# Optimization experiments

Measured on AMD Instinct MI355X. Metric: run time of the kernel, lower is better.

The kernel has to match this reference:

```python
import jax, jax.numpy as jnp
import numpy as np

E, D, H, O, K = 8, 1024, 4096, 1024, 2
N = 4096


def setup_inputs() -> dict:
    key = jax.random.key(0)
    ks = jax.random.split(key, 8)
    s_in = 1.0 / np.sqrt(D)
    s_h = 1.0 / np.sqrt(H)
    return {
        "x": jax.random.normal(ks[0], (N, D), dtype=jnp.float32),
        "W1": jax.random.uniform(ks[1], (E, D, H), jnp.float32, -s_in, s_in),
        "b1": jax.random.uniform(ks[2], (E, H), jnp.float32, -s_in, s_in),
        "W2": jax.random.uniform(ks[3], (E, H, O), jnp.float32, -s_h, s_h),
        "b2": jax.random.uniform(ks[4], (E, O), jnp.float32, -s_h, s_h),
        "Wg": jax.random.uniform(ks[5], (D, E), jnp.float32, -s_in, s_in),
        "bg": jax.random.uniform(ks[6], (E,), jnp.float32, -s_in, s_in),
    }


def reference(x, W1, b1, W2, b2, Wg, bg):
    # gate: [N, E] -> top-k logits and expert ids
    gate_logits = x @ Wg + bg
    topv, topi = jax.lax.top_k(gate_logits, K)          # [N, K]
    weights = jax.nn.softmax(topv, axis=-1)             # softmax over the k selected logits

    # dense all-expert MLP, then gather the selected experts per token
    h = jax.nn.relu(jnp.einsum("nd,edh->enh", x, W1) + b1[:, None, :])  # [E, N, H]
    y = jnp.einsum("enh,eho->eno", h, W2) + b2[:, None, :]              # [E, N, O]

    sel = y[topi, jnp.arange(N)[:, None]]               # [N, K, O]
    return jnp.sum(weights[..., None] * sel, axis=1)    # [N, O]
```

## Files before the change

### kernel.cpp

```cpp
#include <hip/hip_runtime.h>
#include <hip/hip_bf16.h>
#include <cstdint>

typedef __bf16 bf16;
typedef bf16 bf16x8 __attribute__((ext_vector_type(8)));
typedef bf16 bf16x4 __attribute__((ext_vector_type(4)));
typedef float f32x4 __attribute__((ext_vector_type(4)));

#define N_TOK 4096
#define DIM   1024
#define HID   4096
#define OUTD  1024
#define NEXP  8

__device__ __forceinline__ void async_copy16(const void* g, void* l) {
  __builtin_amdgcn_global_load_lds(
      (const __attribute__((address_space(1))) void*)g,
      (__attribute__((address_space(3))) void*)l, 16, 0, 0);
}

__global__ __launch_bounds__(256) void gate_kernel(
    const float* __restrict__ x, const float* __restrict__ Wg,
    const float* __restrict__ bg, int* __restrict__ topE, float* __restrict__ topW)
{
  int wave = threadIdx.x >> 6, lane = threadIdx.x & 63;
  int t = blockIdx.x * 4 + wave;
  float acc[8];
#pragma unroll
  for (int e = 0; e < 8; ++e) acc[e] = 0.f;
  const float* xrow = x + (size_t)t * DIM;
#pragma unroll
  for (int i = 0; i < DIM / 64; ++i) {
    int d = i * 64 + lane;
    float xv = xrow[d];
    float4 w0 = *(const float4*)(Wg + d * 8);
    float4 w1 = *(const float4*)(Wg + d * 8 + 4);
    acc[0] += xv * w0.x; acc[1] += xv * w0.y; acc[2] += xv * w0.z; acc[3] += xv * w0.w;
    acc[4] += xv * w1.x; acc[5] += xv * w1.y; acc[6] += xv * w1.z; acc[7] += xv * w1.w;
  }
#pragma unroll
  for (int off = 32; off > 0; off >>= 1) {
#pragma unroll
    for (int e = 0; e < 8; ++e) acc[e] += __shfl_xor(acc[e], off, 64);
  }
  if (lane == 0) {
    float l[8];
#pragma unroll
    for (int e = 0; e < 8; ++e) l[e] = acc[e] + bg[e];
    int e1 = 0;
#pragma unroll
    for (int e = 1; e < 8; ++e) if (l[e] > l[e1]) e1 = e;
    int e2 = (e1 == 0) ? 1 : 0;
#pragma unroll
    for (int e = 0; e < 8; ++e) if (e != e1 && l[e] > l[e2]) e2 = e;
    float w1 = 1.f / (1.f + __expf(l[e2] - l[e1]));
    topE[t * 2] = e1; topE[t * 2 + 1] = e2;
    topW[t * 2] = w1; topW[t * 2 + 1] = 1.f - w1;
  }
}

__global__ __launch_bounds__(256) void build_lists(
    const int* __restrict__ topE, const float* __restrict__ topW,
    int* __restrict__ cnt, int* __restrict__ tok_list, float* __restrict__ w_list,
    int* __restrict__ inv)
{
  __shared__ int lcnt[8], lbase[8];
  int tid = threadIdx.x;
  if (tid < 8) lcnt[tid] = 0;
  __syncthreads();
  int t = blockIdx.x * 256 + tid;
  int e1 = topE[2 * t], e2 = topE[2 * t + 1];
  float w1 = topW[2 * t], w2 = topW[2 * t + 1];
  int p1 = atomicAdd(&lcnt[e1], 1);
  int p2 = atomicAdd(&lcnt[e2], 1);
  __syncthreads();
  if (tid < 8) lbase[tid] = atomicAdd(&cnt[tid], lcnt[tid]);
  __syncthreads();
  int i1 = e1 * N_TOK + lbase[e1] + p1;
  int i2 = e2 * N_TOK + lbase[e2] + p2;
  tok_list[i1] = t; w_list[i1] = w1;
  tok_list[i2] = t; w_list[i2] = w2;
  inv[2 * t] = i1;
  inv[2 * t + 1] = i2;
}

__global__ void scan_kernel(const int* __restrict__ cnt, int* __restrict__ base)
{
  if (threadIdx.x == 0) {
    int s = 0;
    for (int e = 0; e < 8; ++e) { base[e] = s; s += cnt[e]; }
    base[8] = s;
  }
}

__global__ __launch_bounds__(256) void gather_cvt(
    const float* __restrict__ x, const int* __restrict__ tok_list,
    const int* __restrict__ base, bf16* __restrict__ xg)
{
  int wave = threadIdx.x >> 6, lane = threadIdx.x & 63;
  int s = blockIdx.x * 4 + wave;
  int e = 0;
#pragma unroll
  for (int i = 1; i < 8; ++i) e += (s >= base[i]);
  int tok = tok_list[e * N_TOK + (s - base[e])];
  const float4* src = (const float4*)(x + (size_t)tok * DIM);
  bf16x4* dst = (bf16x4*)(xg + (size_t)s * DIM);
#pragma unroll
  for (int i = 0; i < DIM / 256; ++i) {
    float4 v = src[i * 64 + lane];
    bf16x4 o;
    o.x = (bf16)v.x; o.y = (bf16)v.y; o.z = (bf16)v.z; o.w = (bf16)v.w;
    dst[i * 64 + lane] = o;
  }
}

__global__ __launch_bounds__(256) void transpose_cvt(
    const float* __restrict__ src, bf16* __restrict__ dst, int R, int C)
{
  __shared__ bf16 tile[64][65];
  int e = blockIdx.z;
  const float* s = src + (size_t)e * R * C;
  bf16* d = dst + (size_t)e * R * C;
  int c0 = blockIdx.x * 64, r0 = blockIdx.y * 64;
  int tid = threadIdx.x;
  int rr = tid >> 4;
  int cc = (tid & 15) * 4;
#pragma unroll
  for (int i = 0; i < 4; ++i) {
    int r = i * 16 + rr;
    float4 v = *(const float4*)(s + (size_t)(r0 + r) * C + c0 + cc);
    tile[cc + 0][r] = (bf16)v.x;
    tile[cc + 1][r] = (bf16)v.y;
    tile[cc + 2][r] = (bf16)v.z;
    tile[cc + 3][r] = (bf16)v.w;
  }
  __syncthreads();
#pragma unroll
  for (int i = 0; i < 4; ++i) {
    int ct = i * 16 + rr;
    bf16x4 o;
    o.x = tile[ct][cc + 0];
    o.y = tile[ct][cc + 1];
    o.z = tile[ct][cc + 2];
    o.w = tile[ct][cc + 3];
    *(bf16x4*)(d + (size_t)(c0 + ct) * R + r0 + cc) = o;
  }
}

__global__ __launch_bounds__(256) void gemm1_kernel(
    const bf16* __restrict__ xg, const bf16* __restrict__ W1t,
    const float* __restrict__ b1, bf16* __restrict__ hbuf,
    const int* __restrict__ cnt, const int* __restrict__ base)
{
  int e = blockIdx.z;
  int M = cnt[e];
  int mt = blockIdx.y;
  if (mt * 128 >= M) return;
  int nt = blockIdx.x;
  int b0 = base[e];

  __shared__ bf16 As[128 * 32];
  __shared__ bf16 Bs[128 * 32];

  int tid = threadIdx.x;
  int wave = tid >> 6, lane = tid & 63;

  int rA0 = wave * 32 + (lane >> 2);
  int rA1 = rA0 + 16;
  int kofs = (lane & 3) * 8;
  int lm0 = min(mt * 128 + rA0, M - 1);
  int lm1 = min(mt * 128 + rA1, M - 1);
  const bf16* gA0 = xg + (size_t)(b0 + lm0) * DIM + kofs;
  const bf16* gA1 = xg + (size_t)(b0 + lm1) * DIM + kofs;
  const bf16* gB0 = W1t + ((size_t)e * HID + nt * 128 + rA0) * DIM + kofs;
  const bf16* gB1 = W1t + ((size_t)e * HID + nt * 128 + rA1) * DIM + kofs;
  bf16* lA0 = As + (wave * 2 + 0) * 512;
  bf16* lA1 = As + (wave * 2 + 1) * 512;
  bf16* lB0 = Bs + (wave * 2 + 0) * 512;
  bf16* lB1 = Bs + (wave * 2 + 1) * 512;

  int wm = wave & 1, wn = wave >> 1;
  int quad = lane >> 4, lr = lane & 15;
  f32x4 acc[4][4] = {};

  for (int kt = 0; kt < DIM / 32; ++kt) {
    int ko = kt * 32;
    async_copy16(gA0 + ko, lA0);
    async_copy16(gA1 + ko, lA1);
    async_copy16(gB0 + ko, lB0);
    async_copy16(gB1 + ko, lB1);
    __syncthreads();
    bf16x8 af[4], bfr[4];
#pragma unroll
    for (int i = 0; i < 4; ++i)
      af[i] = *(const bf16x8*)(As + (wm * 64 + i * 16 + lr) * 32 + quad * 8);
#pragma unroll
    for (int j = 0; j < 4; ++j)
      bfr[j] = *(const bf16x8*)(Bs + (wn * 64 + j * 16 + lr) * 32 + quad * 8);
#pragma unroll
    for (int i = 0; i < 4; ++i)
#pragma unroll
      for (int j = 0; j < 4; ++j)
        acc[i][j] = __builtin_amdgcn_mfma_f32_16x16x32_bf16(af[i], bfr[j], acc[i][j], 0, 0, 0);
    __syncthreads();
  }

#pragma unroll
  for (int j = 0; j < 4; ++j) {
    int col = nt * 128 + wn * 64 + j * 16 + lr;
    float bias = b1[e * HID + col];
#pragma unroll
    for (int i = 0; i < 4; ++i) {
#pragma unroll
      for (int r = 0; r < 4; ++r) {
        int lm = mt * 128 + wm * 64 + i * 16 + quad * 4 + r;
        if (lm < M) {
          float v = acc[i][j][r] + bias;
          hbuf[(size_t)(b0 + lm) * HID + col] = (bf16)fmaxf(v, 0.f);
        }
      }
    }
  }
}

__global__ __launch_bounds__(256) void gemm2_kernel(
    const bf16* __restrict__ hbuf, const bf16* __restrict__ W2t,
    const float* __restrict__ b2, float* __restrict__ ybufA, float* __restrict__ ybufB,
    const int* __restrict__ cnt, const int* __restrict__ base)
{
  int e = blockIdx.z;
  int M = cnt[e];
  int mt = blockIdx.y;
  if (mt * 128 >= M) return;
  int nt = blockIdx.x;
  int b0 = base[e];

  __shared__ bf16 As[128 * 32];
  __shared__ bf16 Bs[128 * 32];

  int tid = threadIdx.x;
  int wave = tid >> 6, lane = tid & 63;

  int rA0 = wave * 32 + (lane >> 2);
  int rA1 = rA0 + 16;
  int kofs = (lane & 3) * 8;
  int lm0 = min(mt * 128 + rA0, M - 1);
  int lm1 = min(mt * 128 + rA1, M - 1);
  const bf16* gA0 = hbuf + (size_t)(b0 + lm0) * HID + kofs;
  const bf16* gA1 = hbuf + (size_t)(b0 + lm1) * HID + kofs;
  const bf16* gB0 = W2t + ((size_t)e * OUTD + nt * 128 + rA0) * HID + kofs;
  const bf16* gB1 = W2t + ((size_t)e * OUTD + nt * 128 + rA1) * HID + kofs;
  bf16* lA0 = As + (wave * 2 + 0) * 512;
  bf16* lA1 = As + (wave * 2 + 1) * 512;
  bf16* lB0 = Bs + (wave * 2 + 0) * 512;
  bf16* lB1 = Bs + (wave * 2 + 1) * 512;

  int wm = wave & 1, wn = wave >> 1;
  int quad = lane >> 4, lr = lane & 15;
  f32x4 acc[4][4] = {};

  for (int kt = 0; kt < HID / 32; ++kt) {
    int ko = kt * 32;
    async_copy16(gA0 + ko, lA0);
    async_copy16(gA1 + ko, lA1);
    async_copy16(gB0 + ko, lB0);
    async_copy16(gB1 + ko, lB1);
    __syncthreads();
    bf16x8 af[4], bfr[4];
#pragma unroll
    for (int i = 0; i < 4; ++i)
      af[i] = *(const bf16x8*)(As + (wm * 64 + i * 16 + lr) * 32 + quad * 8);
#pragma unroll
    for (int j = 0; j < 4; ++j)
      bfr[j] = *(const bf16x8*)(Bs + (wn * 64 + j * 16 + lr) * 32 + quad * 8);
#pragma unroll
    for (int i = 0; i < 4; ++i)
#pragma unroll
      for (int j = 0; j < 4; ++j)
        acc[i][j] = __builtin_amdgcn_mfma_f32_16x16x32_bf16(af[i], bfr[j], acc[i][j], 0, 0, 0);
    __syncthreads();
  }

#pragma unroll
  for (int j = 0; j < 4; ++j) {
    int col = nt * 128 + wn * 64 + j * 16 + lr;
    float bias = b2[e * OUTD + col];
#pragma unroll
    for (int i = 0; i < 4; ++i) {
#pragma unroll
      for (int r = 0; r < 4; ++r) {
        int lm = mt * 128 + wm * 64 + i * 16 + quad * 4 + r;
        if (lm < M) {
          int slot = b0 + lm;
          float* yr = (slot < 4096) ? (ybufA + (size_t)slot * OUTD)
                                    : (ybufB + (size_t)(slot - 4096) * OUTD);
          yr[col] = acc[i][j][r] + bias;
        }
      }
    }
  }
}

__global__ __launch_bounds__(256) void combine_kernel(
    const float* __restrict__ ybufA, const float* __restrict__ ybufB,
    const int* __restrict__ inv, const float* __restrict__ topW,
    const int* __restrict__ base, float* __restrict__ out)
{
  int wave = threadIdx.x >> 6, lane = threadIdx.x & 63;
  int t = blockIdx.x * 4 + wave;
  int i0 = inv[2 * t], i1 = inv[2 * t + 1];
  float w0 = topW[2 * t], w1 = topW[2 * t + 1];
  int s0 = base[i0 >> 12] + (i0 & (N_TOK - 1));
  int s1 = base[i1 >> 12] + (i1 & (N_TOK - 1));
  const float4* r0 = (const float4*)((s0 < 4096) ? (ybufA + (size_t)s0 * OUTD)
                                                 : (ybufB + (size_t)(s0 - 4096) * OUTD));
  const float4* r1 = (const float4*)((s1 < 4096) ? (ybufA + (size_t)s1 * OUTD)
                                                 : (ybufB + (size_t)(s1 - 4096) * OUTD));
  float4* o = (float4*)(out + (size_t)t * OUTD);
#pragma unroll
  for (int i = 0; i < OUTD / 256; ++i) {
    float4 a = r0[i * 64 + lane];
    float4 b = r1[i * 64 + lane];
    float4 c;
    c.x = w0 * a.x + w1 * b.x;
    c.y = w0 * a.y + w1 * b.y;
    c.z = w0 * a.z + w1 * b.z;
    c.w = w0 * a.w + w1 * b.w;
    o[i * 64 + lane] = c;
  }
}

extern "C" void kernel_launch(void* const* d_in, const int* in_sizes, int n_in,
                              void* d_out, int out_size, void* d_ws, size_t ws_size,
                              hipStream_t stream)
{
  (void)in_sizes; (void)n_in; (void)ws_size; (void)out_size;
  const float* x  = (const float*)d_in[0];
  const float* W1 = (const float*)d_in[1];
  const float* b1 = (const float*)d_in[2];
  const float* W2 = (const float*)d_in[3];
  const float* b2 = (const float*)d_in[4];
  const float* Wg = (const float*)d_in[5];
  const float* bg = (const float*)d_in[6];
  float* out = (float*)d_out;

  char* ws = (char*)d_ws;
  int*   tok_list = (int*)(ws + 0);
  float* w_list   = (float*)(ws + 131072);
  int*   topE     = (int*)(ws + 262144);
  float* topW     = (float*)(ws + 294912);
  int*   cnt      = (int*)(ws + 327680);
  int*   base     = (int*)(ws + 327744);
  int*   inv      = (int*)(ws + 327808);
  bf16*  xg    = (bf16*)(ws + 393216);
  bf16*  W1t   = (bf16*)(ws + 17170432);
  bf16*  hbuf  = (bf16*)(ws + 84279296);
  bf16*  W2t   = (bf16*)(ws + 393216);
  float* ybufA = (float*)(ws + 67502080);
  float* ybufB = (float*)(ws + 151388160);

  hipMemsetAsync(cnt, 0, 64, stream);

  gate_kernel<<<dim3(N_TOK / 4), 256, 0, stream>>>(x, Wg, bg, topE, topW);
  build_lists<<<dim3(N_TOK / 256), 256, 0, stream>>>(topE, topW, cnt, tok_list, w_list, inv);
  scan_kernel<<<dim3(1), 64, 0, stream>>>(cnt, base);
  gather_cvt<<<dim3(2 * N_TOK / 4), 256, 0, stream>>>(x, tok_list, base, xg);
  transpose_cvt<<<dim3(HID / 64, DIM / 64, NEXP), 256, 0, stream>>>(W1, W1t, DIM, HID);
  gemm1_kernel<<<dim3(HID / 128, N_TOK / 128, NEXP), 256, 0, stream>>>(xg, W1t, b1, hbuf, cnt, base);
  transpose_cvt<<<dim3(OUTD / 64, HID / 64, NEXP), 256, 0, stream>>>(W2, W2t, HID, OUTD);
  gemm2_kernel<<<dim3(OUTD / 128, N_TOK / 128, NEXP), 256, 0, stream>>>(hbuf, W2t, b2, ybufA, ybufB, cnt, base);
  combine_kernel<<<dim3(N_TOK / 4), 256, 0, stream>>>(ybufA, ybufB, inv, topW, base, out);
}
```

Before: 588.4 us.

## Enlarge GEMM tiles to 256x128 with 8 waves and XCD-aware block remap

Both expert GEMMs now use 512-thread blocks computing 256x128 output tiles, so each B (weight) tile loaded into LDS is reused across twice as many token rows. A 1D grid is remapped so consecutive block IDs are spread across the 8 XCDs in contiguous chunks, aiming for better L2 locality. The transpose kernel's LDS tile is padded to 68 columns so the readback can be a single vector load. Larger tiles mean fewer blocks and more idle rows when an expert's token count is not a multiple of 256, and 512-thread blocks may lower occupancy.

```diff
diff --git a/kernel.cpp b/kernel.cpp
--- a/kernel.cpp
+++ b/kernel.cpp
@@ -117,7 +117,7 @@
 __global__ __launch_bounds__(256) void transpose_cvt(
     const float* __restrict__ src, bf16* __restrict__ dst, int R, int C)
 {
-  __shared__ bf16 tile[64][65];
+  __shared__ bf16 tile[64][68];
   int e = blockIdx.z;
   const float* s = src + (size_t)e * R * C;
   bf16* d = dst + (size_t)e * R * C;
@@ -138,48 +138,48 @@
 #pragma unroll
   for (int i = 0; i < 4; ++i) {
     int ct = i * 16 + rr;
-    bf16x4 o;
-    o.x = tile[ct][cc + 0];
-    o.y = tile[ct][cc + 1];
-    o.z = tile[ct][cc + 2];
-    o.w = tile[ct][cc + 3];
+    bf16x4 o = *(const bf16x4*)&tile[ct][cc];
     *(bf16x4*)(d + (size_t)(c0 + ct) * R + r0 + cc) = o;
   }
 }
 
-__global__ __launch_bounds__(256) void gemm1_kernel(
+#define G1_NT (HID / 128)
+#define G1_MT (N_TOK / 256)
+__global__ __launch_bounds__(512) void gemm1_kernel(
     const bf16* __restrict__ xg, const bf16* __restrict__ W1t,
     const float* __restrict__ b1, bf16* __restrict__ hbuf,
     const int* __restrict__ cnt, const int* __restrict__ base)
 {
-  int e = blockIdx.z;
+  const int NWG = NEXP * G1_MT * G1_NT;
+  int bid = (int)blockIdx.x;
+  int wgs = (bid & 7) * (NWG / 8) + (bid >> 3);
+  int mt = wgs & (G1_MT - 1);
+  int nt = (wgs >> 4) & (G1_NT - 1);
+  int e  = wgs >> 9;
   int M = cnt[e];
-  int mt = blockIdx.y;
-  if (mt * 128 >= M) return;
-  int nt = blockIdx.x;
+  if (mt * 256 >= M) return;
   int b0 = base[e];
 
-  __shared__ bf16 As[128 * 32];
+  __shared__ bf16 As[256 * 32];
   __shared__ bf16 Bs[128 * 32];
 
   int tid = threadIdx.x;
   int wave = tid >> 6, lane = tid & 63;
-
-  int rA0 = wave * 32 + (lane >> 2);
-  int rA1 = rA0 + 16;
-  int kofs = (lane & 3) * 8;
-  int lm0 = min(mt * 128 + rA0, M - 1);
-  int lm1 = min(mt * 128 + rA1, M - 1);
-  const bf16* gA0 = xg + (size_t)(b0 + lm0) * DIM + kofs;
-  const bf16* gA1 = xg + (size_t)(b0 + lm1) * DIM + kofs;
-  const bf16* gB0 = W1t + ((size_t)e * HID + nt * 128 + rA0) * DIM + kofs;
-  const bf16* gB1 = W1t + ((size_t)e * HID + nt * 128 + rA1) * DIM + kofs;
-  bf16* lA0 = As + (wave * 2 + 0) * 512;
-  bf16* lA1 = As + (wave * 2 + 1) * 512;
-  bf16* lB0 = Bs + (wave * 2 + 0) * 512;
-  bf16* lB1 = Bs + (wave * 2 + 1) * 512;
-
-  int wm = wave & 1, wn = wave >> 1;
+  int rq = lane >> 2;
+  int kq = (lane & 3) * 8;
+
+  int rowA0 = wave * 32 + rq;
+  int rowA1 = rowA0 + 16;
+  int lm0 = min(mt * 256 + rowA0, M - 1);
+  int lm1 = min(mt * 256 + rowA1, M - 1);
+  const bf16* gA0 = xg + (size_t)(b0 + lm0) * DIM + kq;
+  const bf16* gA1 = xg + (size_t)(b0 + lm1) * DIM + kq;
+  const bf16* gB  = W1t + ((size_t)e * HID + nt * 128 + wave * 16 + rq) * DIM + kq;
+  bf16* lA0 = As + (wave * 32) * 32;
+  bf16* lA1 = As + (wave * 32 + 16) * 32;
+  bf16* lB  = Bs + (wave * 16) * 32;
+
+  int wm = wave & 3, wn = wave >> 2;
   int quad = lane >> 4, lr = lane & 15;
   f32x4 acc[4][4] = {};
 
@@ -187,8 +187,7 @@
     int ko = kt * 32;
     async_copy16(gA0 + ko, lA0);
     async_copy16(gA1 + ko, lA1);
-    async_copy16(gB0 + ko, lB0);
-    async_copy16(gB1 + ko, lB1);
+    async_copy16(gB + ko, lB);
     __syncthreads();
     bf16x8 af[4], bfr[4];
 #pragma unroll
@@ -213,49 +212,53 @@
     for (int i = 0; i < 4; ++i) {
 #pragma unroll
       for (int r = 0; r < 4; ++r) {
-        int lm = mt * 128 + wm * 64 + i * 16 + quad * 4 + r;
-        if (lm < M) {
+        int gm = mt * 256 + wm * 64 + i * 16 + quad * 4 + r;
+        if (gm < M) {
           float v = acc[i][j][r] + bias;
-          hbuf[(size_t)(b0 + lm) * HID + col] = (bf16)fmaxf(v, 0.f);
+          hbuf[(size_t)(b0 + gm) * HID + col] = (bf16)fmaxf(v, 0.f);
         }
       }
     }
   }
 }
 
-__global__ __launch_bounds__(256) void gemm2_kernel(
+#define G2_NT (OUTD / 128)
+#define G2_MT (N_TOK / 256)
+__global__ __launch_bounds__(512) void gemm2_kernel(
     const bf16* __restrict__ hbuf, const bf16* __restrict__ W2t,
     const float* __restrict__ b2, float* __restrict__ ybufA, float* __restrict__ ybufB,
     const int* __restrict__ cnt, const int* __restrict__ base)
 {
-  int e = blockIdx.z;
+  const int NWG = NEXP * G2_MT * G2_NT;
+  int bid = (int)blockIdx.x;
+  int wgs = (bid & 7) * (NWG / 8) + (bid >> 3);
+  int mt = wgs & (G2_MT - 1);
+  int nt = (wgs >> 4) & (G2_NT - 1);
+  int e  = wgs >> 7;
   int M = cnt[e];
-  int mt = blockIdx.y;
-  if (mt * 128 >= M) return;
-  int nt = blockIdx.x;
+  if (mt * 256 >= M) return;
   int b0 = base[e];
 
-  __shared__ bf16 As[128 * 32];
+  __shared__ bf16 As[256 * 32];
   __shared__ bf16 Bs[128 * 32];
 
   int tid = threadIdx.x;
   int wave = tid >> 6, lane = tid & 63;
-
-  int rA0 = wave * 32 + (lane >> 2);
-  int rA1 = rA0 + 16;
-  int kofs = (lane & 3) * 8;
-  int lm0 = min(mt * 128 + rA0, M - 1);
-  int lm1 = min(mt * 128 + rA1, M - 1);
-  const bf16* gA0 = hbuf + (size_t)(b0 + lm0) * HID + kofs;
-  const bf16* gA1 = hbuf + (size_t)(b0 + lm1) * HID + kofs;
-  const bf16* gB0 = W2t + ((size_t)e * OUTD + nt * 128 + rA0) * HID + kofs;
-  const bf16* gB1 = W2t + ((size_t)e * OUTD + nt * 128 + rA1) * HID + kofs;
-  bf16* lA0 = As + (wave * 2 + 0) * 512;
-  bf16* lA1 = As + (wave * 2 + 1) * 512;
-  bf16* lB0 = Bs + (wave * 2 + 0) * 512;
-  bf16* lB1 = Bs + (wave * 2 + 1) * 512;
-
-  int wm = wave & 1, wn = wave >> 1;
+  int rq = lane >> 2;
+  int kq = (lane & 3) * 8;
+
+  int rowA0 = wave * 32 + rq;
+  int rowA1 = rowA0 + 16;
+  int lm0 = min(mt * 256 + rowA0, M - 1);
+  int lm1 = min(mt * 256 + rowA1, M - 1);
+  const bf16* gA0 = hbuf + (size_t)(b0 + lm0) * HID + kq;
+  const bf16* gA1 = hbuf + (size_t)(b0 + lm1) * HID + kq;
+  const bf16* gB  = W2t + ((size_t)e * OUTD + nt * 128 + wave * 16 + rq) * HID + kq;
+  bf16* lA0 = As + (wave * 32) * 32;
+  bf16* lA1 = As + (wave * 32 + 16) * 32;
+  bf16* lB  = Bs + (wave * 16) * 32;
+
+  int wm = wave & 3, wn = wave >> 2;
   int quad = lane >> 4, lr = lane & 15;
   f32x4 acc[4][4] = {};
 
@@ -263,8 +266,7 @@
     int ko = kt * 32;
     async_copy16(gA0 + ko, lA0);
     async_copy16(gA1 + ko, lA1);
-    async_copy16(gB0 + ko, lB0);
-    async_copy16(gB1 + ko, lB1);
+    async_copy16(gB + ko, lB);
     __syncthreads();
     bf16x8 af[4], bfr[4];
 #pragma unroll
@@ -289,9 +291,9 @@
     for (int i = 0; i < 4; ++i) {
 #pragma unroll
       for (int r = 0; r < 4; ++r) {
-        int lm = mt * 128 + wm * 64 + i * 16 + quad * 4 + r;
-        if (lm < M) {
-          int slot = b0 + lm;
+        int gm = mt * 256 + wm * 64 + i * 16 + quad * 4 + r;
+        if (gm < M) {
+          int slot = b0 + gm;
           float* yr = (slot < 4096) ? (ybufA + (size_t)slot * OUTD)
                                     : (ybufB + (size_t)(slot - 4096) * OUTD);
           yr[col] = acc[i][j][r] + bias;
@@ -366,8 +368,8 @@
   scan_kernel<<<dim3(1), 64, 0, stream>>>(cnt, base);
   gather_cvt<<<dim3(2 * N_TOK / 4), 256, 0, stream>>>(x, tok_list, base, xg);
   transpose_cvt<<<dim3(HID / 64, DIM / 64, NEXP), 256, 0, stream>>>(W1, W1t, DIM, HID);
-  gemm1_kernel<<<dim3(HID / 128, N_TOK / 128, NEXP), 256, 0, stream>>>(xg, W1t, b1, hbuf, cnt, base);
+  gemm1_kernel<<<dim3(NEXP * G1_MT * G1_NT), 512, 0, stream>>>(xg, W1t, b1, hbuf, cnt, base);
   transpose_cvt<<<dim3(OUTD / 64, HID / 64, NEXP), 256, 0, stream>>>(W2, W2t, HID, OUTD);
-  gemm2_kernel<<<dim3(OUTD / 128, N_TOK / 128, NEXP), 256, 0, stream>>>(hbuf, W2t, b2, ybufA, ybufB, cnt, base);
+  gemm2_kernel<<<dim3(NEXP * G2_MT * G2_NT), 512, 0, stream>>>(hbuf, W2t, b2, ybufA, ybufB, cnt, base);
   combine_kernel<<<dim3(N_TOK / 4), 256, 0, stream>>>(ybufA, ybufB, inv, topW, base, out);
 }
```

New measurement: 638.6 us. 1.09x slower.
